# Optimization experiments

Measured on AMD Instinct MI355X. Metric: run time of the kernel, lower is better.

The kernel has to match this reference:

```python
import jax, jax.numpy as jnp
import numpy as np

B, C, T = 32, 64, 2500
SFREQ = 250
KW_S = 0.5
K = int(KW_S * SFREQ)          # 125-tap wavelet kernel
F = 10                          # n_freqs_init
OCT_MIN, OCT_MAX = 0.0, 3.0
N_OUT = 2
HID = 8
VEC = C * (C + 1) // 2          # 2080 upper-tri vectorization dim
FEAT = F * VEC                  # 20800
EPS = 1e-5


def setup_inputs() -> dict:
    key = jax.random.key(0)
    ks = jax.random.split(key, 4)
    X = jax.random.normal(ks[0], (B, C, T), jnp.float32)
    # wavelet params (octave-scaled), as in Green.__init__ with random_f_init=False
    foi = jnp.linspace(OCT_MIN, OCT_MAX, F).astype(jnp.float32)
    fwhm = -jnp.linspace(OCT_MIN - 1.0, OCT_MAX - 1.0, F).astype(jnp.float32)
    shrink = jnp.float32(-3.0)                       # pre-sigmoid shrinkage
    brn_w = jnp.ones((VEC,), jnp.float32)            # BatchReNorm scale (rebias=False)
    bn1_g = jnp.ones((FEAT,), jnp.float32)
    bn1_b = jnp.zeros((FEAT,), jnp.float32)
    W1 = jax.random.normal(ks[1], (HID, FEAT), jnp.float32) / np.sqrt(FEAT)
    b1 = jnp.zeros((HID,), jnp.float32)
    bn2_g = jnp.ones((HID,), jnp.float32)
    bn2_b = jnp.zeros((HID,), jnp.float32)
    W2 = jax.random.normal(ks[2], (N_OUT, HID), jnp.float32) / np.sqrt(HID)
    b2 = jnp.zeros((N_OUT,), jnp.float32)
    return dict(X=X, foi=foi, fwhm=fwhm, shrink=shrink, brn_w=brn_w,
                bn1_g=bn1_g, bn1_b=bn1_b, W1=W1, b1=b1,
                bn2_g=bn2_g, bn2_b=bn2_b, W2=W2, b2=b2)


def reference(X, foi, fwhm, shrink, brn_w, bn1_g, bn1_b, W1, b1, bn2_g, bn2_b, W2, b2):
    # ---- WaveletConv: Gabor (Morlet) bank, octave scaling, VALID conv, stride 1 ----
    t = (jnp.arange(K, dtype=jnp.float32) - (K - 1) / 2.0) / SFREQ   # (K,) seconds
    f_hz = 2.0 ** foi                                                # (F,)
    fwhm_s = 2.0 ** fwhm                                             # (F,) seconds
    sigma = fwhm_s / (2.0 * jnp.sqrt(2.0 * jnp.log(2.0)))
    env = jnp.exp(-0.5 * (t[None, :] / sigma[:, None]) ** 2)         # (F,K)
    env = env / jnp.sum(env, axis=1, keepdims=True)                  # unit-mass envelope
    phase = 2.0 * jnp.pi * f_hz[:, None] * t[None, :]
    kern = jnp.concatenate([env * jnp.cos(phase), env * jnp.sin(phase)], 0)[:, None, :]  # (2F,1,K)
    Xr = X.reshape(B * C, 1, T)
    Y = jax.lax.conv_general_dilated(Xr, kern, (1,), 'VALID',
                                     dimension_numbers=('NCH', 'OIH', 'NCH'))  # (B*C,2F,Tc)
    Tc = Y.shape[-1]                                 # T - K + 1 = 2376
    Y = Y.reshape(B, C, 2 * F, Tc)
    Zr, Zi = Y[:, :, :F], Y[:, :, F:]                # real/imag parts, (B,C,F,Tc)
    # ---- real covariance pooling: Re(Z Z^H)/Tc per (batch, freq) ----
    Ccov = (jnp.einsum('bcft,bdft->bfcd', Zr, Zr)
            + jnp.einsum('bcft,bdft->bfcd', Zi, Zi)) / Tc            # (B,F,C,C)
    # ---- learnable shrinkage toward scaled identity ----
    alpha = jax.nn.sigmoid(shrink)
    mu = jnp.mean(jnp.diagonal(Ccov, axis1=-2, axis2=-1), axis=-1)   # (B,F)
    Cs = (1.0 - alpha) * Ccov + alpha * mu[..., None, None] * jnp.eye(C, dtype=Ccov.dtype)
    # ---- LogEig: batched matrix log + upper-tri vectorization (sqrt2 off-diag) ----
    w, V = jnp.linalg.eigh(Cs)
    logC = jnp.einsum('bfij,bfj,bfkj->bfik', V, jnp.log(w), V)       # (B,F,C,C)
    iu, ju = jnp.triu_indices(C)
    scale = jnp.where(iu == ju, 1.0, jnp.sqrt(2.0)).astype(logC.dtype)
    vec = logC[..., iu, ju] * scale                                  # (B,F,VEC)
    # ---- BatchReNorm (scale only, stats over batch and freq axes) ----
    m = jnp.mean(vec, (0, 1))
    v = jnp.var(vec, (0, 1))
    vec = (vec - m) / jnp.sqrt(v + EPS) * brn_w
    # ---- head: BN -> Linear -> GELU(exact) -> BN -> Linear (dropout = eval/identity) ----
    h = vec.reshape(B, FEAT)
    h = (h - h.mean(0)) / jnp.sqrt(h.var(0) + EPS) * bn1_g + bn1_b
    h = h @ W1.T + b1
    h = jax.nn.gelu(h, approximate=False)
    h = (h - h.mean(0)) / jnp.sqrt(h.var(0) + EPS) * bn2_g + bn2_b
    return h @ W2.T + b2
```

## Files before the change

### kernel.cpp

```cpp
#include <hip/hip_runtime.h>
#include <math.h>

#define NSWEEP 12

#define WS_T16 0
#define WS_IU  2048
#define WS_JU  4128
#define WS_MU  6208
#define WS_SC  8288
#define WS_ACC 10368
#define WS_COV 16384
#define WS_VEC (16384 + 320*4096)
#define WS_Z   1994752

typedef _Float16 f16x8 __attribute__((ext_vector_type(8)));
typedef float f32x16 __attribute__((ext_vector_type(16)));

union H8 { int4 i; f16x8 h; };
union HP { uint32_t u; _Float16 h[2]; };

__device__ inline f32x16 zero16() {
    f32x16 z;
#pragma unroll
    for (int r = 0; r < 16; r++) z[r] = 0.0f;
    return z;
}

__global__ void k0_build(const float* __restrict__ foi, const float* __restrict__ fwhm,
                         _Float16* __restrict__ T16,
                         int* __restrict__ iu, int* __restrict__ ju) {
    __shared__ float env[128];
    __shared__ float ssum;
    int tid = threadIdx.x;
    for (int u = tid; u < 2080; u += 256) {
        int i = 0, off = 0;
        while (off + (64 - i) <= u) { off += (64 - i); i++; }
        iu[u] = i;
        ju[u] = i + (u - off);
    }
    for (int idx = tid; idx < 32 * 128; idx += 256) T16[idx] = (_Float16)0.0f;
    __syncthreads();
    const float inv_sfreq = 1.0f / 250.0f;
    for (int f = 0; f < 10; f++) {
        float fhz = exp2f(foi[f]);
        float sig = exp2f(fwhm[f]) / (2.0f * sqrtf(2.0f * logf(2.0f)));
        if (tid < 128) {
            float e = 0.0f;
            if (tid < 125) {
                float t = ((float)tid - 62.0f) * inv_sfreq;
                float z = t / sig;
                e = expf(-0.5f * z * z);
            }
            env[tid] = e;
        }
        __syncthreads();
        if (tid == 0) {
            float s = 0.0f;
            for (int k = 0; k < 125; k++) s += env[k];
            ssum = s;
        }
        __syncthreads();
        if (tid < 125) {
            float e = env[tid] / ssum;
            float t = ((float)tid - 62.0f) * inv_sfreq;
            float ph = 6.283185307179586f * fhz * t;
            T16[f * 128 + tid] = (_Float16)(e * cosf(ph));
            T16[(10 + f) * 128 + tid] = (_Float16)(e * sinf(ph));
        }
        __syncthreads();
    }
}

__global__ __launch_bounds__(256) void kconv(const float* __restrict__ X,
                                             const _Float16* __restrict__ T16,
                                             _Float16* __restrict__ Zbuf,
                                             int t0chunk, int Tpad, int subs) {
    __shared__ __align__(16) uint32_t P[64 * 256];
    int tid = threadIdx.x;
    int b = blockIdx.x / subs;
    int sub = blockIdx.x - b * subs;
    int tbase = t0chunk + sub * 128;
    const float* Xb = X + b * (64 * 2500);
    bool fastblk = (tbase + 256 < 2500);
    for (int task = tid; task < 64 * 64; task += 256) {
        int c = task >> 6, grp = task & 63;
        int t = tbase + grp * 4;
        const float* src = Xb + c * 2500 + t;
        float x0, x1, x2, x3, x4;
        if (fastblk) {
            float4 v = *(const float4*)src;
            x0 = v.x; x1 = v.y; x2 = v.z; x3 = v.w; x4 = src[4];
        } else {
            x0 = (t + 0 < 2500) ? src[0] : 0.0f;
            x1 = (t + 1 < 2500) ? src[1] : 0.0f;
            x2 = (t + 2 < 2500) ? src[2] : 0.0f;
            x3 = (t + 3 < 2500) ? src[3] : 0.0f;
            x4 = (t + 4 < 2500) ? src[4] : 0.0f;
        }
        HP p0, p1, p2, p3;
        p0.h[0] = (_Float16)x0; p0.h[1] = (_Float16)x1;
        p1.h[0] = (_Float16)x1; p1.h[1] = (_Float16)x2;
        p2.h[0] = (_Float16)x2; p2.h[1] = (_Float16)x3;
        p3.h[0] = (_Float16)x3; p3.h[1] = (_Float16)x4;
        uint4 up; up.x = p0.u; up.y = p1.u; up.z = p2.u; up.w = p3.u;
        *(uint4*)&P[c * 256 + grp * 4] = up;
    }
    __syncthreads();
    int lane = tid & 63;
    int w = tid >> 6;
    int n = lane & 31, g = lane >> 5;
    H8 a[8];
#pragma unroll
    for (int ks = 0; ks < 8; ks++)
        a[ks].i = *(const int4*)(T16 + n * 128 + ks * 16 + g * 8);
    int tw = w * 32;
    int colg = tbase + tw + n;
    bool colok = (colg < 2376);
    int tloc = sub * 128 + tw + n;
    int zb0 = b * 1280;
    for (int c = 0; c < 64; c++) {
        f32x16 acc = zero16();
        const uint32_t* Pc = &P[c * 256 + tw + n + 8 * g];
#pragma unroll
        for (int ks = 0; ks < 8; ks++) {
            H8 bv;
            bv.i.x = (int)Pc[16 * ks + 0];
            bv.i.y = (int)Pc[16 * ks + 2];
            bv.i.z = (int)Pc[16 * ks + 4];
            bv.i.w = (int)Pc[16 * ks + 6];
            acc = __builtin_amdgcn_mfma_f32_32x32x16_f16(a[ks].h, bv.h, acc, 0, 0, 0);
        }
        if (colok) {
            int zb = zb0 + c;
#pragma unroll
            for (int r = 0; r < 16; r++) {
                int row = (r & 3) + 8 * (r >> 2) + 4 * g;
                if (row < 20)
                    Zbuf[(zb + row * 64) * Tpad + tloc] = (_Float16)acc[r];
            }
        }
    }
}

__global__ __launch_bounds__(256) void kcov(const _Float16* __restrict__ Zbuf,
                                            float* __restrict__ cov,
                                            int t0chunk, int Tcur, int Tpad) {
    __shared__ __align__(16) _Float16 Zs[2][64 * 100];
    int tid = threadIdx.x;
    int lane = tid & 63, w = tid >> 6;
    int n = lane & 31, g = lane >> 5;
    int bf = blockIdx.x;
    int b = bf / 10, f = bf - b * 10;
    const _Float16* Zr = Zbuf + (size_t)((b * 20 + f) * 64) * Tpad;
    const _Float16* Zi = Zbuf + (size_t)((b * 20 + 10 + f) * 64) * Tpad;
    int ti = w >> 1, tj = w & 1;
    f32x16 acc = zero16();
    int limit = min(Tcur, 2376 - t0chunk);
    int nsub = (limit + 95) / 96;
    for (int sc = 0; sc < nsub; sc++) {
        int tl0 = sc * 96;
        __syncthreads();
        for (int task = tid; task < 1536; task += 256) {
            int arr = task / 768;
            int rem = task - arr * 768;
            int c = rem / 12;
            int o = (rem - c * 12) * 8;
            int tg = tl0 + o;
            const _Float16* src = (arr ? Zi : Zr) + c * Tpad + tg;
            H8 v;
            if (tg + 8 <= limit) {
                v.i = *(const int4*)src;
            } else {
#pragma unroll
                for (int j2 = 0; j2 < 8; j2++)
                    v.h[j2] = (tg + j2 < limit) ? src[j2] : (_Float16)0.0f;
            }
            *(int2*)&Zs[arr][c * 100 + o] = make_int2(v.i.x, v.i.y);
            *(int2*)&Zs[arr][c * 100 + o + 4] = make_int2(v.i.z, v.i.w);
        }
        __syncthreads();
        int ra = (32 * ti + n) * 100 + g * 8;
        int rb = (32 * tj + n) * 100 + g * 8;
#pragma unroll
        for (int arr = 0; arr < 2; arr++) {
#pragma unroll
            for (int ks = 0; ks < 6; ks++) {
                const _Float16* pa = &Zs[arr][ra + ks * 16];
                const _Float16* pb = &Zs[arr][rb + ks * 16];
                int2 a0 = *(const int2*)pa;
                int2 a1 = *(const int2*)(pa + 4);
                int2 b0 = *(const int2*)pb;
                int2 b1 = *(const int2*)(pb + 4);
                H8 av, bv;
                av.i = make_int4(a0.x, a0.y, a1.x, a1.y);
                bv.i = make_int4(b0.x, b0.y, b1.x, b1.y);
                acc = __builtin_amdgcn_mfma_f32_32x32x16_f16(av.h, bv.h, acc, 0, 0, 0);
            }
        }
    }
    float* covbf = cov + bf * 4096;
    int col = 32 * tj + n;
#pragma unroll
    for (int r = 0; r < 16; r++) {
        int row = 32 * ti + (r & 3) + 8 * (r >> 2) + 4 * g;
        covbf[row * 64 + col] += acc[r];
    }
}

__global__ __launch_bounds__(64) void keja(float* __restrict__ cov,
                                           const float* __restrict__ shrink,
                                           float* __restrict__ dvec,
                                           float* __restrict__ dmu) {
    int s = threadIdx.x;
    int bf = blockIdx.x;
    float* C = cov + bf * 4096;
    float w[64];
#pragma unroll
    for (int r = 0; r < 64; r++) w[r] = C[r * 64 + s];
    float ts = C[s * 65];
#pragma unroll
    for (int m = 1; m < 64; m <<= 1) ts += __shfl_xor(ts, m, 64);
    float mu = ts * (1.0f / (64.0f * 2376.0f));
    float alpha = 1.0f / (1.0f + expf(-shrink[0]));
    float scl = (1.0f - alpha) / (2376.0f * fmaxf(mu, 1e-30f));
#pragma unroll
    for (int r = 0; r < 64; r++) {
        float v = w[r] * scl;
        if (r == s) v += alpha;
        w[r] = v;
    }
    for (int sweep = 0; sweep < NSWEEP; sweep++) {
        float n0 = 0, n1 = 0, n2 = 0, n3 = 0;
#pragma unroll
        for (int r = 0; r < 64; r += 4) {
            n0 = fmaf(w[r], w[r], n0);
            n1 = fmaf(w[r + 1], w[r + 1], n1);
            n2 = fmaf(w[r + 2], w[r + 2], n2);
            n3 = fmaf(w[r + 3], w[r + 3], n3);
        }
        float nrm = (n0 + n1) + (n2 + n3);
        for (int m = 1; m < 64; m++) {
            int addr = (s ^ m) << 2;
            float q[64];
#pragma unroll
            for (int r = 0; r < 64; r++)
                q[r] = __int_as_float(__builtin_amdgcn_ds_bpermute(addr, __float_as_int(w[r])));
            float d0 = 0, d1 = 0, d2 = 0, d3 = 0;
#pragma unroll
            for (int r = 0; r < 64; r += 4) {
                d0 = fmaf(w[r], q[r], d0);
                d1 = fmaf(w[r + 1], q[r + 1], d1);
                d2 = fmaf(w[r + 2], q[r + 2], d2);
                d3 = fmaf(w[r + 3], q[r + 3], d3);
            }
            float dpq = (d0 + d1) + (d2 + d3);
            float pn = __int_as_float(__builtin_amdgcn_ds_bpermute(addr, __float_as_int(nrm)));
            int h = 31 - __builtin_clz((unsigned)m);
            bool top = (((s >> h) & 1) == 0);
            float dpp = top ? nrm : pn;
            float dqq = top ? pn : nrm;
            bool rot = (dpq * dpq > 1e-13f * dpp * dqq);
            float tau = (dqq - dpp) / (2.0f * dpq);
            float tt = 1.0f / (fabsf(tau) + sqrtf(1.0f + tau * tau));
            if (tau < 0.0f) tt = -tt;
            if (!rot) tt = 0.0f;
            float cc = rsqrtf(1.0f + tt * tt);
            float ssn = tt * cc;
            float sg = top ? -ssn : ssn;
#pragma unroll
            for (int r = 0; r < 64; r++)
                w[r] = cc * w[r] + sg * q[r];
            nrm = fmaf(top ? -tt : tt, dpq, nrm);
        }
    }
    float n0 = 0, n1 = 0, n2 = 0, n3 = 0;
#pragma unroll
    for (int r = 0; r < 64; r += 4) {
        n0 = fmaf(w[r], w[r], n0);
        n1 = fmaf(w[r + 1], w[r + 1], n1);
        n2 = fmaf(w[r + 2], w[r + 2], n2);
        n3 = fmaf(w[r + 3], w[r + 3], n3);
    }
    float nrm = (n0 + n1) + (n2 + n3);
    float d = 0.5f * logf(nrm) / nrm;
#pragma unroll
    for (int r = 0; r < 64; r++) C[r * 64 + s] = w[r];
    dvec[bf * 64 + s] = d;
    if (s == 0) dmu[bf] = logf(fmaxf(mu, 1e-30f));
}

__global__ __launch_bounds__(256) void kvec(const float* __restrict__ W,
                                            const float* __restrict__ dvec,
                                            const float* __restrict__ dmu,
                                            const int* __restrict__ iu,
                                            const int* __restrict__ ju,
                                            float* __restrict__ vec) {
    __shared__ float WL[64 * 68];
    __shared__ float WD[64 * 68];
    __shared__ float ds[64];
    int tid = threadIdx.x;
    int bf = blockIdx.x;
    const float* Wb = W + bf * 4096;
    if (tid < 64) ds[tid] = dvec[bf * 64 + tid];
    __syncthreads();
    for (int idx = tid; idx < 4096; idx += 256) {
        int i = idx >> 6, c = idx & 63;
        float v = Wb[idx];
        WL[i * 68 + c] = v;
        WD[i * 68 + c] = v * ds[c];
    }
    __syncthreads();
    float logmu = dmu[bf];
    float* out = vec + bf * 2080;
    for (int u = tid; u < 2080; u += 256) {
        int i = iu[u], j = ju[u];
        const float* a = &WD[i * 68];
        const float* b = &WL[j * 68];
        float s0 = 0, s1 = 0, s2 = 0, s3 = 0;
#pragma unroll
        for (int k = 0; k < 64; k += 16) {
            float4 a0 = *(const float4*)(a + k);
            float4 b0 = *(const float4*)(b + k);
            float4 a1 = *(const float4*)(a + k + 4);
            float4 b1 = *(const float4*)(b + k + 4);
            float4 a2 = *(const float4*)(a + k + 8);
            float4 b2 = *(const float4*)(b + k + 8);
            float4 a3 = *(const float4*)(a + k + 12);
            float4 b3 = *(const float4*)(b + k + 12);
            s0 = fmaf(a0.x, b0.x, fmaf(a0.y, b0.y, fmaf(a0.z, b0.z, fmaf(a0.w, b0.w, s0))));
            s1 = fmaf(a1.x, b1.x, fmaf(a1.y, b1.y, fmaf(a1.z, b1.z, fmaf(a1.w, b1.w, s1))));
            s2 = fmaf(a2.x, b2.x, fmaf(a2.y, b2.y, fmaf(a2.z, b2.z, fmaf(a2.w, b2.w, s2))));
            s3 = fmaf(a3.x, b3.x, fmaf(a3.y, b3.y, fmaf(a3.z, b3.z, fmaf(a3.w, b3.w, s3))));
        }
        float ssm = (s0 + s1) + (s2 + s3);
        if (i == j) ssm += logmu;
        else ssm *= 1.4142135623730951f;
        out[u] = ssm;
    }
}

__global__ void k3a_stats(const float* __restrict__ vec, const float* __restrict__ brn_w,
                          float* __restrict__ m_u, float* __restrict__ sc_u) {
    int u = blockIdx.x * 256 + threadIdx.x;
    if (u >= 2080) return;
    float s1 = 0.0f, s2 = 0.0f;
    for (int bfi = 0; bfi < 320; bfi++) {
        float x = vec[bfi * 2080 + u];
        s1 += x; s2 += x * x;
    }
    float m = s1 * (1.0f / 320.0f);
    float v = s2 * (1.0f / 320.0f) - m * m;
    m_u[u] = m;
    sc_u[u] = brn_w[u] * rsqrtf(v + 1e-5f);
}

__global__ __launch_bounds__(256) void k3b_bn1mm(const float* __restrict__ vec,
                                                 const float* __restrict__ m_u,
                                                 const float* __restrict__ sc_u,
                                                 const float* __restrict__ g1,
                                                 const float* __restrict__ bb1,
                                                 const float* __restrict__ W1,
                                                 float* __restrict__ acc) {
    __shared__ float hbuf[256 * 33];
    __shared__ float wbuf[8 * 256];
    int tid = threadIdx.x;
    int j = blockIdx.x * 256 + tid;
    bool act = (j < 20800);
    int f = act ? (j / 2080) : 0;
    int u = act ? (j % 2080) : 0;
    float mm = act ? m_u[u] : 0.0f;
    float sc = act ? sc_u[u] : 0.0f;
    float xv[32];
    float s1 = 0.0f, s2 = 0.0f;
    for (int b = 0; b < 32; b++) {
        float x = act ? ((vec[(b * 10 + f) * 2080 + u] - mm) * sc) : 0.0f;
        xv[b] = x;
        s1 += x; s2 += x * x;
    }
    float m1 = s1 * (1.0f / 32.0f);
    float inv1 = rsqrtf(s2 * (1.0f / 32.0f) - m1 * m1 + 1e-5f);
    float gg = act ? g1[j] : 0.0f;
    float bb = act ? bb1[j] : 0.0f;
    for (int b = 0; b < 32; b++)
        hbuf[tid * 33 + b] = (xv[b] - m1) * inv1 * gg + bb;
    for (int hid = 0; hid < 8; hid++)
        wbuf[hid * 256 + tid] = act ? W1[hid * 20800 + j] : 0.0f;
    __syncthreads();
    int b = tid >> 3, hid = tid & 7;
    float ssm = 0.0f;
    for (int jj = 0; jj < 256; jj++)
        ssm += hbuf[jj * 33 + b] * wbuf[hid * 256 + jj];
    atomicAdd(&acc[b * 8 + hid], ssm);
}

__global__ void k4_final(const float* __restrict__ acc, const float* __restrict__ b1,
                         const float* __restrict__ bn2g, const float* __restrict__ bn2b,
                         const float* __restrict__ W2, const float* __restrict__ b2,
                         float* __restrict__ out) {
    __shared__ float gl[256];
    __shared__ float m2[8], i2[8];
    int tid = threadIdx.x;
    int b = tid >> 3, hid = tid & 7;
    float x = acc[tid] + b1[hid];
    float ge = 0.5f * x * (1.0f + erff(x * 0.7071067811865476f));
    gl[tid] = ge;
    __syncthreads();
    if (tid < 8) {
        float s1 = 0.0f, s2 = 0.0f;
        for (int bb = 0; bb < 32; bb++) {
            float v = gl[bb * 8 + tid];
            s1 += v; s2 += v * v;
        }
        float mm = s1 * (1.0f / 32.0f);
        m2[tid] = mm;
        i2[tid] = rsqrtf(s2 * (1.0f / 32.0f) - mm * mm + 1e-5f);
    }
    __syncthreads();
    float h2 = (ge - m2[hid]) * i2[hid] * bn2g[hid] + bn2b[hid];
    gl[tid] = h2;
    __syncthreads();
    if (tid < 64) {
        int bo = tid >> 1, o = tid & 1;
        float ssm = b2[o];
        for (int hh = 0; hh < 8; hh++) ssm += gl[bo * 8 + hh] * W2[o * 8 + hh];
        out[bo * 2 + o] = ssm;
    }
}

extern "C" void kernel_launch(void* const* d_in, const int* in_sizes, int n_in,
                              void* d_out, int out_size, void* d_ws, size_t ws_size,
                              hipStream_t stream) {
    const float* X     = (const float*)d_in[0];
    const float* foi   = (const float*)d_in[1];
    const float* fwhm  = (const float*)d_in[2];
    const float* shrink= (const float*)d_in[3];
    const float* brn_w = (const float*)d_in[4];
    const float* bn1_g = (const float*)d_in[5];
    const float* bn1_b = (const float*)d_in[6];
    const float* W1    = (const float*)d_in[7];
    const float* b1    = (const float*)d_in[8];
    const float* bn2_g = (const float*)d_in[9];
    const float* bn2_b = (const float*)d_in[10];
    const float* W2    = (const float*)d_in[11];
    const float* b2    = (const float*)d_in[12];

    float* ws    = (float*)d_ws;
    _Float16* T16= (_Float16*)(ws + WS_T16);
    int*   iu    = (int*)(ws + WS_IU);
    int*   ju    = (int*)(ws + WS_JU);
    float* m_u   = ws + WS_MU;
    float* sc_u  = ws + WS_SC;
    float* acc   = ws + WS_ACC;
    float* cov   = ws + WS_COV;
    float* vec   = ws + WS_VEC;
    _Float16* Zbuf = (_Float16*)(ws + WS_Z);
    float* dvec  = (float*)(ws + WS_Z);
    float* dmuv  = dvec + 320 * 64;

    size_t zavail = (ws_size > (size_t)WS_Z * 4) ? ws_size - (size_t)WS_Z * 4 : 0;
    const int cand[6] = {2432, 1152, 768, 384, 256, 128};
    int Tchunk = 128;
    for (int i = 0; i < 6; i++) {
        if (81920ull * (size_t)cand[i] <= zavail) { Tchunk = cand[i]; break; }
    }

    hipMemsetAsync(cov, 0, 320 * 4096 * sizeof(float), stream);
    hipMemsetAsync(acc, 0, 256 * sizeof(float), stream);

    k0_build<<<1, 256, 0, stream>>>(foi, fwhm, T16, iu, ju);
    for (int t0 = 0; t0 < 2376; t0 += Tchunk) {
        int Tcur = min(Tchunk, 2376 - t0);
        int subs = (Tcur + 127) / 128;
        kconv<<<32 * subs, 256, 0, stream>>>(X, T16, Zbuf, t0, Tchunk, subs);
        kcov<<<320, 256, 0, stream>>>(Zbuf, cov, t0, Tcur, Tchunk);
    }
    keja<<<320, 64, 0, stream>>>(cov, shrink, dvec, dmuv);
    kvec<<<320, 256, 0, stream>>>(cov, dvec, dmuv, iu, ju, vec);
    k3a_stats<<<9, 256, 0, stream>>>(vec, brn_w, m_u, sc_u);
    k3b_bn1mm<<<82, 256, 0, stream>>>(vec, m_u, sc_u, bn1_g, bn1_b, W1, acc);
    k4_final<<<1, 256, 0, stream>>>(acc, b1, bn2_g, bn2_b, W2, b2, (float*)d_out);
}
```

Before: 845.6 us.

## Process two matrices per wavefront in Jacobi eigensolver and cut sweeps

The one-sided Jacobi kernel now handles two covariance matrices per 64-thread block, interleaving their bpermute exchanges and rotations to raise instruction-level parallelism, and launches 160 blocks instead of 320. The sweep count also drops from 12 to 10, which removes about a sixth of the rotation work. Two 64-float arrays plus two exchange buffers per thread greatly raise register pressure and may cause spills. Fewer blocks may also leave compute units idle on a 256-CU device, and fewer sweeps risk lower eigen-decomposition accuracy.

```diff
diff --git a/kernel.cpp b/kernel.cpp
--- a/kernel.cpp
+++ b/kernel.cpp
@@ -1,7 +1,7 @@
 #include <hip/hip_runtime.h>
 #include <math.h>
 
-#define NSWEEP 12
+#define NSWEEP 10
 
 #define WS_T16 0
 #define WS_IU  2048
@@ -207,86 +207,122 @@
     }
 }
 
-__global__ __launch_bounds__(64) void keja(float* __restrict__ cov,
-                                           const float* __restrict__ shrink,
-                                           float* __restrict__ dvec,
-                                           float* __restrict__ dmu) {
+__global__ __launch_bounds__(64, 1) void keja2(float* __restrict__ cov,
+                                               const float* __restrict__ shrink,
+                                               float* __restrict__ dvec,
+                                               float* __restrict__ dmu) {
     int s = threadIdx.x;
-    int bf = blockIdx.x;
-    float* C = cov + bf * 4096;
-    float w[64];
-#pragma unroll
-    for (int r = 0; r < 64; r++) w[r] = C[r * 64 + s];
-    float ts = C[s * 65];
-#pragma unroll
-    for (int m = 1; m < 64; m <<= 1) ts += __shfl_xor(ts, m, 64);
-    float mu = ts * (1.0f / (64.0f * 2376.0f));
+    int bfA = blockIdx.x * 2;
+    int bfB = bfA + 1;
+    float* CA = cov + bfA * 4096;
+    float* CB = cov + bfB * 4096;
+    float wA[64], wB[64];
+#pragma unroll
+    for (int r = 0; r < 64; r++) wA[r] = CA[r * 64 + s];
+#pragma unroll
+    for (int r = 0; r < 64; r++) wB[r] = CB[r * 64 + s];
     float alpha = 1.0f / (1.0f + expf(-shrink[0]));
-    float scl = (1.0f - alpha) / (2376.0f * fmaxf(mu, 1e-30f));
+    float tsA = CA[s * 65];
+    float tsB = CB[s * 65];
+#pragma unroll
+    for (int m = 1; m < 64; m <<= 1) {
+        tsA += __shfl_xor(tsA, m, 64);
+        tsB += __shfl_xor(tsB, m, 64);
+    }
+    float muA = tsA * (1.0f / (64.0f * 2376.0f));
+    float muB = tsB * (1.0f / (64.0f * 2376.0f));
+    float sclA = (1.0f - alpha) / (2376.0f * fmaxf(muA, 1e-30f));
+    float sclB = (1.0f - alpha) / (2376.0f * fmaxf(muB, 1e-30f));
 #pragma unroll
     for (int r = 0; r < 64; r++) {
-        float v = w[r] * scl;
-        if (r == s) v += alpha;
-        w[r] = v;
+        float vA = wA[r] * sclA;
+        float vB = wB[r] * sclB;
+        if (r == s) { vA += alpha; vB += alpha; }
+        wA[r] = vA; wB[r] = vB;
     }
     for (int sweep = 0; sweep < NSWEEP; sweep++) {
-        float n0 = 0, n1 = 0, n2 = 0, n3 = 0;
-#pragma unroll
-        for (int r = 0; r < 64; r += 4) {
-            n0 = fmaf(w[r], w[r], n0);
-            n1 = fmaf(w[r + 1], w[r + 1], n1);
-            n2 = fmaf(w[r + 2], w[r + 2], n2);
-            n3 = fmaf(w[r + 3], w[r + 3], n3);
-        }
-        float nrm = (n0 + n1) + (n2 + n3);
+        float a0 = 0, a1 = 0, b0 = 0, b1 = 0;
+#pragma unroll
+        for (int r = 0; r < 64; r += 2) {
+            a0 = fmaf(wA[r], wA[r], a0);
+            a1 = fmaf(wA[r + 1], wA[r + 1], a1);
+            b0 = fmaf(wB[r], wB[r], b0);
+            b1 = fmaf(wB[r + 1], wB[r + 1], b1);
+        }
+        float nrmA = a0 + a1;
+        float nrmB = b0 + b1;
         for (int m = 1; m < 64; m++) {
             int addr = (s ^ m) << 2;
-            float q[64];
+            float qA[64], qB[64];
 #pragma unroll
             for (int r = 0; r < 64; r++)
-                q[r] = __int_as_float(__builtin_amdgcn_ds_bpermute(addr, __float_as_int(w[r])));
-            float d0 = 0, d1 = 0, d2 = 0, d3 = 0;
-#pragma unroll
-            for (int r = 0; r < 64; r += 4) {
-                d0 = fmaf(w[r], q[r], d0);
-                d1 = fmaf(w[r + 1], q[r + 1], d1);
-                d2 = fmaf(w[r + 2], q[r + 2], d2);
-                d3 = fmaf(w[r + 3], q[r + 3], d3);
+                qA[r] = __int_as_float(__builtin_amdgcn_ds_bpermute(addr, __float_as_int(wA[r])));
+#pragma unroll
+            for (int r = 0; r < 64; r++)
+                qB[r] = __int_as_float(__builtin_amdgcn_ds_bpermute(addr, __float_as_int(wB[r])));
+            float dA0 = 0, dA1 = 0, dB0 = 0, dB1 = 0;
+#pragma unroll
+            for (int r = 0; r < 64; r += 2) {
+                dA0 = fmaf(wA[r], qA[r], dA0);
+                dA1 = fmaf(wA[r + 1], qA[r + 1], dA1);
+                dB0 = fmaf(wB[r], qB[r], dB0);
+                dB1 = fmaf(wB[r + 1], qB[r + 1], dB1);
             }
-            float dpq = (d0 + d1) + (d2 + d3);
-            float pn = __int_as_float(__builtin_amdgcn_ds_bpermute(addr, __float_as_int(nrm)));
+            float dpqA = dA0 + dA1;
+            float dpqB = dB0 + dB1;
+            float pnA = __int_as_float(__builtin_amdgcn_ds_bpermute(addr, __float_as_int(nrmA)));
+            float pnB = __int_as_float(__builtin_amdgcn_ds_bpermute(addr, __float_as_int(nrmB)));
             int h = 31 - __builtin_clz((unsigned)m);
             bool top = (((s >> h) & 1) == 0);
-            float dpp = top ? nrm : pn;
-            float dqq = top ? pn : nrm;
-            bool rot = (dpq * dpq > 1e-13f * dpp * dqq);
-            float tau = (dqq - dpp) / (2.0f * dpq);
-            float tt = 1.0f / (fabsf(tau) + sqrtf(1.0f + tau * tau));
-            if (tau < 0.0f) tt = -tt;
-            if (!rot) tt = 0.0f;
-            float cc = rsqrtf(1.0f + tt * tt);
-            float ssn = tt * cc;
-            float sg = top ? -ssn : ssn;
-#pragma unroll
-            for (int r = 0; r < 64; r++)
-                w[r] = cc * w[r] + sg * q[r];
-            nrm = fmaf(top ? -tt : tt, dpq, nrm);
-        }
-    }
-    float n0 = 0, n1 = 0, n2 = 0, n3 = 0;
-#pragma unroll
-    for (int r = 0; r < 64; r += 4) {
-        n0 = fmaf(w[r], w[r], n0);
-        n1 = fmaf(w[r + 1], w[r + 1], n1);
-        n2 = fmaf(w[r + 2], w[r + 2], n2);
-        n3 = fmaf(w[r + 3], w[r + 3], n3);
-    }
-    float nrm = (n0 + n1) + (n2 + n3);
-    float d = 0.5f * logf(nrm) / nrm;
-#pragma unroll
-    for (int r = 0; r < 64; r++) C[r * 64 + s] = w[r];
-    dvec[bf * 64 + s] = d;
-    if (s == 0) dmu[bf] = logf(fmaxf(mu, 1e-30f));
+            float dppA = top ? nrmA : pnA;
+            float dqqA = top ? pnA : nrmA;
+            float dppB = top ? nrmB : pnB;
+            float dqqB = top ? pnB : nrmB;
+            bool rotA = (dpqA * dpqA > 1e-13f * dppA * dqqA);
+            bool rotB = (dpqB * dpqB > 1e-13f * dppB * dqqB);
+            float tauA = (dqqA - dppA) / (2.0f * dpqA);
+            float tauB = (dqqB - dppB) / (2.0f * dpqB);
+            float ttA = 1.0f / (fabsf(tauA) + sqrtf(1.0f + tauA * tauA));
+            float ttB = 1.0f / (fabsf(tauB) + sqrtf(1.0f + tauB * tauB));
+            if (tauA < 0.0f) ttA = -ttA;
+            if (tauB < 0.0f) ttB = -ttB;
+            if (!rotA) ttA = 0.0f;
+            if (!rotB) ttB = 0.0f;
+            float ccA = rsqrtf(1.0f + ttA * ttA);
+            float ccB = rsqrtf(1.0f + ttB * ttB);
+            float ssA = ttA * ccA;
+            float ssB = ttB * ccB;
+            float sgA = top ? -ssA : ssA;
+            float sgB = top ? -ssB : ssB;
+#pragma unroll
+            for (int r = 0; r < 64; r++) {
+                wA[r] = fmaf(ccA, wA[r], sgA * qA[r]);
+                wB[r] = fmaf(ccB, wB[r], sgB * qB[r]);
+            }
+            nrmA = fmaf(top ? -ttA : ttA, dpqA, nrmA);
+            nrmB = fmaf(top ? -ttB : ttB, dpqB, nrmB);
+        }
+    }
+    float a0 = 0, a1 = 0, b0 = 0, b1 = 0;
+#pragma unroll
+    for (int r = 0; r < 64; r += 2) {
+        a0 = fmaf(wA[r], wA[r], a0);
+        a1 = fmaf(wA[r + 1], wA[r + 1], a1);
+        b0 = fmaf(wB[r], wB[r], b0);
+        b1 = fmaf(wB[r + 1], wB[r + 1], b1);
+    }
+    float nrmA = a0 + a1;
+    float nrmB = b0 + b1;
+#pragma unroll
+    for (int r = 0; r < 64; r++) CA[r * 64 + s] = wA[r];
+#pragma unroll
+    for (int r = 0; r < 64; r++) CB[r * 64 + s] = wB[r];
+    dvec[bfA * 64 + s] = 0.5f * logf(nrmA) / nrmA;
+    dvec[bfB * 64 + s] = 0.5f * logf(nrmB) / nrmB;
+    if (s == 0) {
+        dmu[bfA] = logf(fmaxf(muA, 1e-30f));
+        dmu[bfB] = logf(fmaxf(muB, 1e-30f));
+    }
 }
 
 __global__ __launch_bounds__(256) void kvec(const float* __restrict__ W,
@@ -474,7 +510,7 @@
         kconv<<<32 * subs, 256, 0, stream>>>(X, T16, Zbuf, t0, Tchunk, subs);
         kcov<<<320, 256, 0, stream>>>(Zbuf, cov, t0, Tcur, Tchunk);
     }
-    keja<<<320, 64, 0, stream>>>(cov, shrink, dvec, dmuv);
+    keja2<<<160, 64, 0, stream>>>(cov, shrink, dvec, dmuv);
     kvec<<<320, 256, 0, stream>>>(cov, dvec, dmuv, iu, ju, vec);
     k3a_stats<<<9, 256, 0, stream>>>(vec, brn_w, m_u, sc_u);
     k3b_bn1mm<<<82, 256, 0, stream>>>(vec, m_u, sc_u, bn1_g, bn1_b, W1, acc);
```

After: 1.705 ms. 102% more time.

## Pipeline Jacobi rotations with double-buffered bpermute and reduce sweep count

Applied to the files above, without the earlier changes.

Restructures the one-sided Jacobi eigensolver so the cross-lane permute of the next partner column is issued while the current rotation is applied, using two register buffers. It also reduces the number of sweeps from 12 to 9 and refreshes the column norm at each sweep boundary. This targets the serial permute latency and the total rotation work, at the risk of lower eigendecomposition accuracy and higher register pressure.

```diff
diff --git a/kernel.cpp b/kernel.cpp
--- a/kernel.cpp
+++ b/kernel.cpp
@@ -1,7 +1,8 @@
 #include <hip/hip_runtime.h>
 #include <math.h>
 
-#define NSWEEP 12
+#define NSWEEP 9
+#define NIT2   ((NSWEEP * 63 + 1) / 2)
 
 #define WS_T16 0
 #define WS_IU  2048
@@ -24,6 +25,10 @@
 #pragma unroll
     for (int r = 0; r < 16; r++) z[r] = 0.0f;
     return z;
+}
+
+__device__ __forceinline__ float bperm(int addr, float v) {
+    return __int_as_float(__builtin_amdgcn_ds_bpermute(addr, __float_as_int(v)));
 }
 
 __global__ void k0_build(const float* __restrict__ foi, const float* __restrict__ fwhm,
@@ -207,10 +212,10 @@
     }
 }
 
-__global__ __launch_bounds__(64) void keja(float* __restrict__ cov,
-                                           const float* __restrict__ shrink,
-                                           float* __restrict__ dvec,
-                                           float* __restrict__ dmu) {
+__global__ __launch_bounds__(64) void keja4(float* __restrict__ cov,
+                                            const float* __restrict__ shrink,
+                                            float* __restrict__ dvec,
+                                            float* __restrict__ dmu) {
     int s = threadIdx.x;
     int bf = blockIdx.x;
     float* C = cov + bf * 4096;
@@ -229,7 +234,9 @@
         if (r == s) v += alpha;
         w[r] = v;
     }
-    for (int sweep = 0; sweep < NSWEEP; sweep++) {
+    float qa[64], qb[64];
+    float nrm;
+    {
         float n0 = 0, n1 = 0, n2 = 0, n3 = 0;
 #pragma unroll
         for (int r = 0; r < 64; r += 4) {
@@ -238,41 +245,71 @@
             n2 = fmaf(w[r + 2], w[r + 2], n2);
             n3 = fmaf(w[r + 3], w[r + 3], n3);
         }
-        float nrm = (n0 + n1) + (n2 + n3);
-        for (int m = 1; m < 64; m++) {
-            int addr = (s ^ m) << 2;
-            float q[64];
-#pragma unroll
-            for (int r = 0; r < 64; r++)
-                q[r] = __int_as_float(__builtin_amdgcn_ds_bpermute(addr, __float_as_int(w[r])));
-            float d0 = 0, d1 = 0, d2 = 0, d3 = 0;
-#pragma unroll
-            for (int r = 0; r < 64; r += 4) {
-                d0 = fmaf(w[r], q[r], d0);
-                d1 = fmaf(w[r + 1], q[r + 1], d1);
-                d2 = fmaf(w[r + 2], q[r + 2], d2);
-                d3 = fmaf(w[r + 3], q[r + 3], d3);
-            }
-            float dpq = (d0 + d1) + (d2 + d3);
-            float pn = __int_as_float(__builtin_amdgcn_ds_bpermute(addr, __float_as_int(nrm)));
-            int h = 31 - __builtin_clz((unsigned)m);
-            bool top = (((s >> h) & 1) == 0);
-            float dpp = top ? nrm : pn;
-            float dqq = top ? pn : nrm;
-            bool rot = (dpq * dpq > 1e-13f * dpp * dqq);
-            float tau = (dqq - dpp) / (2.0f * dpq);
-            float tt = 1.0f / (fabsf(tau) + sqrtf(1.0f + tau * tau));
-            if (tau < 0.0f) tt = -tt;
-            if (!rot) tt = 0.0f;
-            float cc = rsqrtf(1.0f + tt * tt);
-            float ssn = tt * cc;
-            float sg = top ? -ssn : ssn;
-#pragma unroll
-            for (int r = 0; r < 64; r++)
-                w[r] = cc * w[r] + sg * q[r];
-            nrm = fmaf(top ? -tt : tt, dpq, nrm);
-        }
-    }
+        nrm = (n0 + n1) + (n2 + n3);
+        int addr0 = (s ^ 1) << 2;
+#pragma unroll
+        for (int r = 0; r < 64; r++) qa[r] = bperm(addr0, w[r]);
+    }
+    int mA = 1;
+#define JROUND(MC, QC, QN, MN)                                                  \
+    {                                                                           \
+        int addrC = (s ^ (MC)) << 2;                                            \
+        float pn = bperm(addrC, nrm);   \
+        float d0 = 0, d1 = 0, d2 = 0, d3 = 0;                                   \
+        _Pragma("unroll")                                                       \
+        for (int r = 0; r < 64; r += 4) {                                       \
+            d0 = fmaf(w[r], QC[r], d0);                                         \
+            d1 = fmaf(w[r + 1], QC[r + 1], d1);                                 \
+            d2 = fmaf(w[r + 2], QC[r + 2], d2);                                 \
+            d3 = fmaf(w[r + 3], QC[r + 3], d3);                                 \
+        }                                                                       \
+        float dpq = (d0 + d1) + (d2 + d3);                                      \
+        int h = 31 - __builtin_clz((unsigned)(MC));                             \
+        bool top = (((s >> h) & 1) == 0);                                       \
+        float dpp = top ? nrm : pn;                                             \
+        float dqq = top ? pn : nrm;                                             \
+        bool rot = (dpq * dpq > 1e-13f * dpp * dqq);                            \
+        float tau = (dqq - dpp) / (2.0f * dpq);                                 \
+        float tt = 1.0f / (fabsf(tau) + sqrtf(1.0f + tau * tau));               \
+        if (tau < 0.0f) tt = -tt;                                               \
+        if (!rot) tt = 0.0f;                                                    \
+        float cc = rsqrtf(1.0f + tt * tt);                                      \
+        float ssn = tt * cc;                                                    \
+        float sg = top ? -ssn : ssn;                                            \
+        int addrN = (s ^ (MN)) << 2;                                            \
+        _Pragma("unroll")                                                       \
+        for (int r = 0; r < 32; r++) w[r] = fmaf(cc, w[r], sg * QC[r]);         \
+        _Pragma("unroll")                                                       \
+        for (int r = 0; r < 32; r++) QN[r] = bperm(addrN, w[r]);                \
+        _Pragma("unroll")                                                       \
+        for (int r = 32; r < 64; r++) w[r] = fmaf(cc, w[r], sg * QC[r]);        \
+        _Pragma("unroll")                                                       \
+        for (int r = 32; r < 64; r++) QN[r] = bperm(addrN, w[r]);               \
+        nrm = fmaf(top ? -tt : tt, dpq, nrm);                                   \
+    }
+#define NORMREFRESH                                                             \
+    {                                                                           \
+        float n0 = 0, n1 = 0, n2 = 0, n3 = 0;                                   \
+        _Pragma("unroll")                                                       \
+        for (int r = 0; r < 64; r += 4) {                                       \
+            n0 = fmaf(w[r], w[r], n0);                                          \
+            n1 = fmaf(w[r + 1], w[r + 1], n1);                                  \
+            n2 = fmaf(w[r + 2], w[r + 2], n2);                                  \
+            n3 = fmaf(w[r + 3], w[r + 3], n3);                                  \
+        }                                                                       \
+        nrm = (n0 + n1) + (n2 + n3);                                            \
+    }
+    for (int it = 0; it < NIT2; it++) {
+        int mB = (mA == 63) ? 1 : mA + 1;
+        JROUND(mA, qa, qb, mB);
+        if (mB == 1) NORMREFRESH;
+        int mC = (mB == 63) ? 1 : mB + 1;
+        JROUND(mB, qb, qa, mC);
+        if (mC == 1) NORMREFRESH;
+        mA = mC;
+    }
+#undef JROUND
+#undef NORMREFRESH
     float n0 = 0, n1 = 0, n2 = 0, n3 = 0;
 #pragma unroll
     for (int r = 0; r < 64; r += 4) {
@@ -281,11 +318,10 @@
         n2 = fmaf(w[r + 2], w[r + 2], n2);
         n3 = fmaf(w[r + 3], w[r + 3], n3);
     }
-    float nrm = (n0 + n1) + (n2 + n3);
-    float d = 0.5f * logf(nrm) / nrm;
+    float nf = (n0 + n1) + (n2 + n3);
 #pragma unroll
     for (int r = 0; r < 64; r++) C[r * 64 + s] = w[r];
-    dvec[bf * 64 + s] = d;
+    dvec[bf * 64 + s] = 0.5f * logf(nf) / nf;
     if (s == 0) dmu[bf] = logf(fmaxf(mu, 1e-30f));
 }
 
@@ -474,7 +510,7 @@
         kconv<<<32 * subs, 256, 0, stream>>>(X, T16, Zbuf, t0, Tchunk, subs);
         kcov<<<320, 256, 0, stream>>>(Zbuf, cov, t0, Tcur, Tchunk);
     }
-    keja<<<320, 64, 0, stream>>>(cov, shrink, dvec, dmuv);
+    keja4<<<320, 64, 0, stream>>>(cov, shrink, dvec, dmuv);
     kvec<<<320, 256, 0, stream>>>(cov, dvec, dmuv, iu, ju, vec);
     k3a_stats<<<9, 256, 0, stream>>>(vec, brn_w, m_u, sc_u);
     k3b_bn1mm<<<82, 256, 0, stream>>>(vec, m_u, sc_u, bn1_g, bn1_b, W1, acc);
```

New measurement: 678.7 us. 19.7% less time.
